# Optimization experiments

Hardware: AMD Instinct MI355X
Metric: run time of the kernel (lower is better)

The kernel has to match this reference:

```python
import jax, jax.numpy as jnp
import numpy as np

STATE_DIM = 4        # per-block state size (rel pos + rel vel, 2D)
N_NEIGH = 64         # neighbors per agent
BATCH = 4096         # observations in the batch (len(x) in torch code)
PHI_H, PHI_OUT = 256, 64
RHO_H, ACTION_DIM = 256, 2
R_AGENT = 0.15
A_MAX = 2.0


def setup_inputs() -> dict:
    key = jax.random.key(0)
    ks = jax.random.split(key, 5)

    def w(k, i, o):
        return jax.random.normal(k, (i, o), jnp.float32) / np.sqrt(i).astype(np.float32)

    x = jax.random.normal(ks[0], (BATCH, (N_NEIGH + 2) * STATE_DIM), jnp.float32)
    return dict(
        x=x,
        phi_w1=w(ks[1], STATE_DIM, PHI_H), phi_b1=jnp.zeros((PHI_H,), jnp.float32),
        phi_w2=w(ks[2], PHI_H, PHI_OUT), phi_b2=jnp.zeros((PHI_OUT,), jnp.float32),
        rho_w1=w(ks[3], PHI_OUT, RHO_H), rho_b1=jnp.zeros((RHO_H,), jnp.float32),
        rho_w2=w(ks[4], RHO_H, ACTION_DIM), rho_b2=jnp.zeros((ACTION_DIM,), jnp.float32),
    )


def reference(x, phi_w1, phi_b1, phi_w2, phi_b2, rho_w1, rho_b1, rho_w2, rho_b2):
    B = x.shape[0]
    blocks = x.reshape(B, -1, STATE_DIM)                 # [B, n_n+2, sd]
    # DeepSet: phi per block, permutation-invariant sum, rho head.
    h = jax.nn.relu(jnp.einsum('bns,sh->bnh', blocks, phi_w1) + phi_b1)
    phi = jnp.einsum('bnh,ho->bno', h, phi_w2) + phi_b2  # [B, n_n+2, phi_out]
    X = phi.sum(axis=1)                                  # [B, phi_out]
    h2 = jax.nn.relu(X @ rho_w1 + rho_b1)
    a = A_MAX * jnp.tanh(h2 @ rho_w2 + rho_b2)           # [B, action_dim]
    # Barrier: neighbor blocks start at block index 2; take first half (positions).
    p = blocks[:, 2:, : STATE_DIM // 2]                  # [B, n_n, 2]
    d = jnp.linalg.norm(p, axis=-1, keepdims=True)       # [B, n_n, 1]
    barrier = jnp.sum(-p / (d - R_AGENT) ** 2, axis=1)   # [B, 2]
    barrier = jax.lax.stop_gradient(barrier)  # torch goes through numpy -> detached
    a = a + barrier
    scale = A_MAX / jnp.max(a)  # torch.max(a_max)/torch.max(a_wbarrier), global max
    return jnp.where(scale < 1.0, a * scale, a)
```

## Files before the change

kernel.cpp:

```cpp
#include <hip/hip_runtime.h>
#include <math.h>


#define NBLK 1024

__global__ __launch_bounds__(256, 4) void bn_row(
    const float* __restrict__ x,
    const float* __restrict__ w1,  const float* __restrict__ b1,
    const float* __restrict__ w2,  const float* __restrict__ b2,
    const float* __restrict__ rw1, const float* __restrict__ rb1,
    const float* __restrict__ rw2, const float* __restrict__ rb2,
    float* __restrict__ out, float* __restrict__ blkmax)
{
    __shared__ __align__(16) float sx[4][268];
    __shared__ __align__(16) float sH[4][264];
    __shared__ float sXp[4][4][68];
    __shared__ __align__(16) float sX[4][68];
    __shared__ float sP4[4][4][2];
    __shared__ float sbar[4][2];
    __shared__ float sa[8];

    const int tid = threadIdx.x;
    const int ln  = tid & 63;
    const int wv  = tid >> 6;
    const int b0  = blockIdx.x * 4;
    const int row = b0 + wv;
    const float4* __restrict__ x4 = (const float4*)(x + (size_t)row * 264);

    float4 xr = x4[ln];
    float4 pv = x4[ln + 2];
    ((float4*)sx[wv])[ln] = xr;
    if (ln >= 62) ((float4*)sx[wv])[ln + 2] = pv;

    float4 w1r0 = ((const float4*)(w1      ))[ln];
    float4 w1r1 = ((const float4*)(w1 + 256))[ln];
    float4 w1r2 = ((const float4*)(w1 + 512))[ln];
    float4 w1r3 = ((const float4*)(w1 + 768))[ln];
    float4 b1r  = ((const float4*)b1)[ln];

    float a0 = 0.f, a1 = 0.f, a2 = 0.f, a3 = 0.f;
    #pragma unroll 4
    for (int n = 0; n < 66; n++) {
        float4 xv = ((const float4*)sx[wv])[n];
        float h0 = b1r.x, h1 = b1r.y, h2 = b1r.z, h3 = b1r.w;
        h0 = fmaf(xv.x, w1r0.x, h0); h1 = fmaf(xv.x, w1r0.y, h1);
        h2 = fmaf(xv.x, w1r0.z, h2); h3 = fmaf(xv.x, w1r0.w, h3);
        h0 = fmaf(xv.y, w1r1.x, h0); h1 = fmaf(xv.y, w1r1.y, h1);
        h2 = fmaf(xv.y, w1r1.z, h2); h3 = fmaf(xv.y, w1r1.w, h3);
        h0 = fmaf(xv.z, w1r2.x, h0); h1 = fmaf(xv.z, w1r2.y, h1);
        h2 = fmaf(xv.z, w1r2.z, h2); h3 = fmaf(xv.z, w1r2.w, h3);
        h0 = fmaf(xv.w, w1r3.x, h0); h1 = fmaf(xv.w, w1r3.y, h1);
        h2 = fmaf(xv.w, w1r3.z, h2); h3 = fmaf(xv.w, w1r3.w, h3);
        a0 += fmaxf(h0, 0.f); a1 += fmaxf(h1, 0.f);
        a2 += fmaxf(h2, 0.f); a3 += fmaxf(h3, 0.f);
    }
    ((float4*)sH[wv])[ln] = make_float4(a0, a1, a2, a3);

    {
        float px = pv.x, py = pv.y;
        float d  = sqrtf(px * px + py * py);
        float t  = d - 0.15f;
        float inv = 1.0f / (t * t);
        float bx = -px * inv, by = -py * inv;
        #pragma unroll
        for (int m = 32; m >= 1; m >>= 1) {
            bx += __shfl_xor(bx, m);
            by += __shfl_xor(by, m);
        }
        if (ln == 0) { sbar[wv][0] = bx; sbar[wv][1] = by; }
    }
    __syncthreads();

    {
        float xp0 = 0.f, xp1 = 0.f, xp2 = 0.f, xp3 = 0.f;
        const float* w2q = w2 + (wv << 12);
        #pragma unroll 2
        for (int i = 0; i < 16; i++) {
            int kb = (wv << 4) + i;
            float4 h0 = ((const float4*)sH[0])[kb];
            float4 h1 = ((const float4*)sH[1])[kb];
            float4 h2 = ((const float4*)sH[2])[kb];
            float4 h3 = ((const float4*)sH[3])[kb];
            float wk0 = w2q[(((i << 2) + 0) << 6) + ln];
            float wk1 = w2q[(((i << 2) + 1) << 6) + ln];
            float wk2 = w2q[(((i << 2) + 2) << 6) + ln];
            float wk3 = w2q[(((i << 2) + 3) << 6) + ln];
            xp0 = fmaf(h0.x, wk0, xp0); xp1 = fmaf(h1.x, wk0, xp1);
            xp2 = fmaf(h2.x, wk0, xp2); xp3 = fmaf(h3.x, wk0, xp3);
            xp0 = fmaf(h0.y, wk1, xp0); xp1 = fmaf(h1.y, wk1, xp1);
            xp2 = fmaf(h2.y, wk1, xp2); xp3 = fmaf(h3.y, wk1, xp3);
            xp0 = fmaf(h0.z, wk2, xp0); xp1 = fmaf(h1.z, wk2, xp1);
            xp2 = fmaf(h2.z, wk2, xp2); xp3 = fmaf(h3.z, wk2, xp3);
            xp0 = fmaf(h0.w, wk3, xp0); xp1 = fmaf(h1.w, wk3, xp1);
            xp2 = fmaf(h2.w, wk3, xp2); xp3 = fmaf(h3.w, wk3, xp3);
        }
        sXp[wv][0][ln] = xp0; sXp[wv][1][ln] = xp1;
        sXp[wv][2][ln] = xp2; sXp[wv][3][ln] = xp3;
    }
    __syncthreads();

    {
        float Xf = sXp[0][wv][ln] + sXp[1][wv][ln]
                 + sXp[2][wv][ln] + sXp[3][wv][ln] + 66.0f * b2[ln];
        sX[wv][ln] = Xf;
    }
    __syncthreads();

    float c0, c1, c2, c3;
    c0 = c1 = c2 = c3 = rb1[tid];
    #pragma unroll 2
    for (int i = 0; i < 16; i++) {
        float4 X0 = ((const float4*)sX[0])[i];
        float4 X1 = ((const float4*)sX[1])[i];
        float4 X2 = ((const float4*)sX[2])[i];
        float4 X3 = ((const float4*)sX[3])[i];
        float r0 = rw1[(((i << 2) + 0) << 8) + tid];
        float r1 = rw1[(((i << 2) + 1) << 8) + tid];
        float r2 = rw1[(((i << 2) + 2) << 8) + tid];
        float r3 = rw1[(((i << 2) + 3) << 8) + tid];
        c0 = fmaf(X0.x, r0, c0); c1 = fmaf(X1.x, r0, c1);
        c2 = fmaf(X2.x, r0, c2); c3 = fmaf(X3.x, r0, c3);
        c0 = fmaf(X0.y, r1, c0); c1 = fmaf(X1.y, r1, c1);
        c2 = fmaf(X2.y, r1, c2); c3 = fmaf(X3.y, r1, c3);
        c0 = fmaf(X0.z, r2, c0); c1 = fmaf(X1.z, r2, c1);
        c2 = fmaf(X2.z, r2, c2); c3 = fmaf(X3.z, r2, c3);
        c0 = fmaf(X0.w, r3, c0); c1 = fmaf(X1.w, r3, c1);
        c2 = fmaf(X2.w, r3, c2); c3 = fmaf(X3.w, r3, c3);
    }
    c0 = fmaxf(c0, 0.f); c1 = fmaxf(c1, 0.f);
    c2 = fmaxf(c2, 0.f); c3 = fmaxf(c3, 0.f);

    {
        float2 r2v = ((const float2*)rw2)[tid];
        float p00 = c0 * r2v.x, p01 = c0 * r2v.y;
        float p10 = c1 * r2v.x, p11 = c1 * r2v.y;
        float p20 = c2 * r2v.x, p21 = c2 * r2v.y;
        float p30 = c3 * r2v.x, p31 = c3 * r2v.y;
        #pragma unroll
        for (int m = 32; m >= 1; m >>= 1) {
            p00 += __shfl_xor(p00, m); p01 += __shfl_xor(p01, m);
            p10 += __shfl_xor(p10, m); p11 += __shfl_xor(p11, m);
            p20 += __shfl_xor(p20, m); p21 += __shfl_xor(p21, m);
            p30 += __shfl_xor(p30, m); p31 += __shfl_xor(p31, m);
        }
        if (ln == 0) {
            sP4[wv][0][0] = p00; sP4[wv][0][1] = p01;
            sP4[wv][1][0] = p10; sP4[wv][1][1] = p11;
            sP4[wv][2][0] = p20; sP4[wv][2][1] = p21;
            sP4[wv][3][0] = p30; sP4[wv][3][1] = p31;
        }
    }
    __syncthreads();

    if (tid < 8) {
        int r = tid >> 1, c = tid & 1;
        float pre = sP4[0][r][c] + sP4[1][r][c] + sP4[2][r][c] + sP4[3][r][c] + rb2[c];
        float a = 2.0f * tanhf(pre) + sbar[r][c];
        out[b0 * 2 + tid] = a;
        sa[tid] = a;
    }
    __syncthreads();
    if (tid == 0) {
        float m = sa[0];
        #pragma unroll
        for (int i = 1; i < 8; i++) m = fmaxf(m, sa[i]);
        blkmax[blockIdx.x] = m;
    }
}

__global__ __launch_bounds__(256) void bn_scale(
    float* __restrict__ out, const float* __restrict__ blkmax)
{
    __shared__ float sm[4];
    const int tid = threadIdx.x;
    const int ln  = tid & 63;
    const int wv  = tid >> 6;

    float m = fmaxf(fmaxf(blkmax[tid], blkmax[tid + 256]),
                    fmaxf(blkmax[tid + 512], blkmax[tid + 768]));
    #pragma unroll
    for (int s = 32; s >= 1; s >>= 1) m = fmaxf(m, __shfl_xor(m, s));
    if (ln == 0) sm[wv] = m;
    __syncthreads();
    float amax = fmaxf(fmaxf(sm[0], sm[1]), fmaxf(sm[2], sm[3]));

    float scale = 2.0f / amax;
    int i = blockIdx.x * 256 + tid;
    float a = out[i];
    out[i] = (scale < 1.0f) ? a * scale : a;
}

extern "C" void kernel_launch(void* const* d_in, const int* in_sizes, int n_in,
                              void* d_out, int out_size, void* d_ws, size_t ws_size,
                              hipStream_t stream) {
    const float* x   = (const float*)d_in[0];
    const float* w1  = (const float*)d_in[1];
    const float* b1  = (const float*)d_in[2];
    const float* w2  = (const float*)d_in[3];
    const float* b2  = (const float*)d_in[4];
    const float* rw1 = (const float*)d_in[5];
    const float* rb1 = (const float*)d_in[6];
    const float* rw2 = (const float*)d_in[7];
    const float* rb2 = (const float*)d_in[8];
    float* out = (float*)d_out;
    float* blkmax = (float*)d_ws;

    bn_row<<<NBLK, 256, 0, stream>>>(x, w1, b1, w2, b2, rw1, rb1, rw2, rb2,
                                     out, blkmax);
    bn_scale<<<8192 / 256, 256, 0, stream>>>(out, blkmax);
}
```

Measured before the change: 90.46 us.

## Split each row's phi loop across two waves, two rows per block

Each block now handles 2 rows instead of 4, and each row's 66-block phi layer-1 loop is split between two waves, with the partial sums combined in shared memory. This doubles the grid to 2048 blocks and raises the occupancy hint, cutting the per-wave serial loop length and the per-thread register footprint. The cost is an extra shared-memory reduction and barrier. The w2, rw1 and rw2 weights are also re-read by twice as many blocks, and the second kernel now reduces 2048 block maxima.

```diff
diff --git a/kernel.cpp b/kernel.cpp
--- a/kernel.cpp
+++ b/kernel.cpp
@@ -2,9 +2,9 @@
 #include <math.h>
 
 
-#define NBLK 1024
-
-__global__ __launch_bounds__(256, 4) void bn_row(
+#define NBLK 2048
+
+__global__ __launch_bounds__(256, 8) void bn_row(
     const float* __restrict__ x,
     const float* __restrict__ w1,  const float* __restrict__ b1,
     const float* __restrict__ w2,  const float* __restrict__ b2,
@@ -12,51 +12,62 @@
     const float* __restrict__ rw2, const float* __restrict__ rb2,
     float* __restrict__ out, float* __restrict__ blkmax)
 {
-    __shared__ __align__(16) float sx[4][268];
-    __shared__ __align__(16) float sH[4][264];
-    __shared__ float sXp[4][4][68];
-    __shared__ __align__(16) float sX[4][68];
-    __shared__ float sP4[4][4][2];
-    __shared__ float sbar[4][2];
-    __shared__ float sa[8];
+    __shared__ __align__(16) float sx[2][268];
+    __shared__ __align__(16) float sHp[4][264];
+    __shared__ __align__(16) float sH[2][264];
+    __shared__ float sXp[4][2][68];
+    __shared__ __align__(16) float sX[2][68];
+    __shared__ float sP4[4][2][2];
+    __shared__ float sbar[2][2];
+    __shared__ float sa[4];
 
     const int tid = threadIdx.x;
     const int ln  = tid & 63;
     const int wv  = tid >> 6;
-    const int b0  = blockIdx.x * 4;
-    const int row = b0 + wv;
+    const int p   = wv & 1;
+    const int rp  = wv >> 1;
+    const int r0  = blockIdx.x * 2;
+    const int row = r0 + rp;
     const float4* __restrict__ x4 = (const float4*)(x + (size_t)row * 264);
 
-    float4 xr = x4[ln];
-    float4 pv = x4[ln + 2];
-    ((float4*)sx[wv])[ln] = xr;
-    if (ln >= 62) ((float4*)sx[wv])[ln + 2] = pv;
+    float4 pv;
+    if (p == 0) {
+        float4 xr = x4[ln];
+        ((float4*)sx[rp])[ln] = xr;
+    } else {
+        pv = x4[ln + 2];
+        if (ln >= 62) ((float4*)sx[rp])[ln + 2] = pv;
+    }
 
     float4 w1r0 = ((const float4*)(w1      ))[ln];
     float4 w1r1 = ((const float4*)(w1 + 256))[ln];
     float4 w1r2 = ((const float4*)(w1 + 512))[ln];
     float4 w1r3 = ((const float4*)(w1 + 768))[ln];
     float4 b1r  = ((const float4*)b1)[ln];
+    __syncthreads();
 
     float a0 = 0.f, a1 = 0.f, a2 = 0.f, a3 = 0.f;
-    #pragma unroll 4
-    for (int n = 0; n < 66; n++) {
-        float4 xv = ((const float4*)sx[wv])[n];
-        float h0 = b1r.x, h1 = b1r.y, h2 = b1r.z, h3 = b1r.w;
-        h0 = fmaf(xv.x, w1r0.x, h0); h1 = fmaf(xv.x, w1r0.y, h1);
-        h2 = fmaf(xv.x, w1r0.z, h2); h3 = fmaf(xv.x, w1r0.w, h3);
-        h0 = fmaf(xv.y, w1r1.x, h0); h1 = fmaf(xv.y, w1r1.y, h1);
-        h2 = fmaf(xv.y, w1r1.z, h2); h3 = fmaf(xv.y, w1r1.w, h3);
-        h0 = fmaf(xv.z, w1r2.x, h0); h1 = fmaf(xv.z, w1r2.y, h1);
-        h2 = fmaf(xv.z, w1r2.z, h2); h3 = fmaf(xv.z, w1r2.w, h3);
-        h0 = fmaf(xv.w, w1r3.x, h0); h1 = fmaf(xv.w, w1r3.y, h1);
-        h2 = fmaf(xv.w, w1r3.z, h2); h3 = fmaf(xv.w, w1r3.w, h3);
-        a0 += fmaxf(h0, 0.f); a1 += fmaxf(h1, 0.f);
-        a2 += fmaxf(h2, 0.f); a3 += fmaxf(h3, 0.f);
-    }
-    ((float4*)sH[wv])[ln] = make_float4(a0, a1, a2, a3);
-
     {
+        const int nbeg = p * 33;
+        #pragma unroll 3
+        for (int j = 0; j < 33; j++) {
+            float4 xv = ((const float4*)sx[rp])[nbeg + j];
+            float h0 = b1r.x, h1 = b1r.y, h2 = b1r.z, h3 = b1r.w;
+            h0 = fmaf(xv.x, w1r0.x, h0); h1 = fmaf(xv.x, w1r0.y, h1);
+            h2 = fmaf(xv.x, w1r0.z, h2); h3 = fmaf(xv.x, w1r0.w, h3);
+            h0 = fmaf(xv.y, w1r1.x, h0); h1 = fmaf(xv.y, w1r1.y, h1);
+            h2 = fmaf(xv.y, w1r1.z, h2); h3 = fmaf(xv.y, w1r1.w, h3);
+            h0 = fmaf(xv.z, w1r2.x, h0); h1 = fmaf(xv.z, w1r2.y, h1);
+            h2 = fmaf(xv.z, w1r2.z, h2); h3 = fmaf(xv.z, w1r2.w, h3);
+            h0 = fmaf(xv.w, w1r3.x, h0); h1 = fmaf(xv.w, w1r3.y, h1);
+            h2 = fmaf(xv.w, w1r3.z, h2); h3 = fmaf(xv.w, w1r3.w, h3);
+            a0 += fmaxf(h0, 0.f); a1 += fmaxf(h1, 0.f);
+            a2 += fmaxf(h2, 0.f); a3 += fmaxf(h3, 0.f);
+        }
+    }
+    ((float4*)sHp[wv])[ln] = make_float4(a0, a1, a2, a3);
+
+    if (p == 1) {
         float px = pv.x, py = pv.y;
         float d  = sqrtf(px * px + py * py);
         float t  = d - 0.15f;
@@ -67,103 +78,87 @@
             bx += __shfl_xor(bx, m);
             by += __shfl_xor(by, m);
         }
-        if (ln == 0) { sbar[wv][0] = bx; sbar[wv][1] = by; }
+        if (ln == 0) { sbar[rp][0] = bx; sbar[rp][1] = by; }
+    }
+    __syncthreads();
+
+    for (int t = tid; t < 512; t += 256) {
+        int r = t >> 8, k = t & 255;
+        sH[r][k] = sHp[2 * r][k] + sHp[2 * r + 1][k];
     }
     __syncthreads();
 
     {
-        float xp0 = 0.f, xp1 = 0.f, xp2 = 0.f, xp3 = 0.f;
+        float xp0 = 0.f, xp1 = 0.f;
         const float* w2q = w2 + (wv << 12);
-        #pragma unroll 2
+        #pragma unroll 4
         for (int i = 0; i < 16; i++) {
             int kb = (wv << 4) + i;
             float4 h0 = ((const float4*)sH[0])[kb];
             float4 h1 = ((const float4*)sH[1])[kb];
-            float4 h2 = ((const float4*)sH[2])[kb];
-            float4 h3 = ((const float4*)sH[3])[kb];
             float wk0 = w2q[(((i << 2) + 0) << 6) + ln];
             float wk1 = w2q[(((i << 2) + 1) << 6) + ln];
             float wk2 = w2q[(((i << 2) + 2) << 6) + ln];
             float wk3 = w2q[(((i << 2) + 3) << 6) + ln];
             xp0 = fmaf(h0.x, wk0, xp0); xp1 = fmaf(h1.x, wk0, xp1);
-            xp2 = fmaf(h2.x, wk0, xp2); xp3 = fmaf(h3.x, wk0, xp3);
             xp0 = fmaf(h0.y, wk1, xp0); xp1 = fmaf(h1.y, wk1, xp1);
-            xp2 = fmaf(h2.y, wk1, xp2); xp3 = fmaf(h3.y, wk1, xp3);
             xp0 = fmaf(h0.z, wk2, xp0); xp1 = fmaf(h1.z, wk2, xp1);
-            xp2 = fmaf(h2.z, wk2, xp2); xp3 = fmaf(h3.z, wk2, xp3);
             xp0 = fmaf(h0.w, wk3, xp0); xp1 = fmaf(h1.w, wk3, xp1);
-            xp2 = fmaf(h2.w, wk3, xp2); xp3 = fmaf(h3.w, wk3, xp3);
         }
         sXp[wv][0][ln] = xp0; sXp[wv][1][ln] = xp1;
-        sXp[wv][2][ln] = xp2; sXp[wv][3][ln] = xp3;
-    }
-    __syncthreads();
-
-    {
-        float Xf = sXp[0][wv][ln] + sXp[1][wv][ln]
-                 + sXp[2][wv][ln] + sXp[3][wv][ln] + 66.0f * b2[ln];
-        sX[wv][ln] = Xf;
-    }
-    __syncthreads();
-
-    float c0, c1, c2, c3;
-    c0 = c1 = c2 = c3 = rb1[tid];
-    #pragma unroll 2
+    }
+    __syncthreads();
+
+    if (wv < 2) {
+        sX[wv][ln] = sXp[0][wv][ln] + sXp[1][wv][ln]
+                   + sXp[2][wv][ln] + sXp[3][wv][ln] + 66.0f * b2[ln];
+    }
+    __syncthreads();
+
+    float c0, c1;
+    c0 = c1 = rb1[tid];
+    #pragma unroll 4
     for (int i = 0; i < 16; i++) {
         float4 X0 = ((const float4*)sX[0])[i];
         float4 X1 = ((const float4*)sX[1])[i];
-        float4 X2 = ((const float4*)sX[2])[i];
-        float4 X3 = ((const float4*)sX[3])[i];
-        float r0 = rw1[(((i << 2) + 0) << 8) + tid];
-        float r1 = rw1[(((i << 2) + 1) << 8) + tid];
-        float r2 = rw1[(((i << 2) + 2) << 8) + tid];
-        float r3 = rw1[(((i << 2) + 3) << 8) + tid];
-        c0 = fmaf(X0.x, r0, c0); c1 = fmaf(X1.x, r0, c1);
-        c2 = fmaf(X2.x, r0, c2); c3 = fmaf(X3.x, r0, c3);
-        c0 = fmaf(X0.y, r1, c0); c1 = fmaf(X1.y, r1, c1);
-        c2 = fmaf(X2.y, r1, c2); c3 = fmaf(X3.y, r1, c3);
-        c0 = fmaf(X0.z, r2, c0); c1 = fmaf(X1.z, r2, c1);
-        c2 = fmaf(X2.z, r2, c2); c3 = fmaf(X3.z, r2, c3);
-        c0 = fmaf(X0.w, r3, c0); c1 = fmaf(X1.w, r3, c1);
-        c2 = fmaf(X2.w, r3, c2); c3 = fmaf(X3.w, r3, c3);
+        float q0 = rw1[(((i << 2) + 0) << 8) + tid];
+        float q1 = rw1[(((i << 2) + 1) << 8) + tid];
+        float q2 = rw1[(((i << 2) + 2) << 8) + tid];
+        float q3 = rw1[(((i << 2) + 3) << 8) + tid];
+        c0 = fmaf(X0.x, q0, c0); c1 = fmaf(X1.x, q0, c1);
+        c0 = fmaf(X0.y, q1, c0); c1 = fmaf(X1.y, q1, c1);
+        c0 = fmaf(X0.z, q2, c0); c1 = fmaf(X1.z, q2, c1);
+        c0 = fmaf(X0.w, q3, c0); c1 = fmaf(X1.w, q3, c1);
     }
     c0 = fmaxf(c0, 0.f); c1 = fmaxf(c1, 0.f);
-    c2 = fmaxf(c2, 0.f); c3 = fmaxf(c3, 0.f);
 
     {
         float2 r2v = ((const float2*)rw2)[tid];
         float p00 = c0 * r2v.x, p01 = c0 * r2v.y;
         float p10 = c1 * r2v.x, p11 = c1 * r2v.y;
-        float p20 = c2 * r2v.x, p21 = c2 * r2v.y;
-        float p30 = c3 * r2v.x, p31 = c3 * r2v.y;
         #pragma unroll
         for (int m = 32; m >= 1; m >>= 1) {
             p00 += __shfl_xor(p00, m); p01 += __shfl_xor(p01, m);
             p10 += __shfl_xor(p10, m); p11 += __shfl_xor(p11, m);
-            p20 += __shfl_xor(p20, m); p21 += __shfl_xor(p21, m);
-            p30 += __shfl_xor(p30, m); p31 += __shfl_xor(p31, m);
         }
         if (ln == 0) {
             sP4[wv][0][0] = p00; sP4[wv][0][1] = p01;
             sP4[wv][1][0] = p10; sP4[wv][1][1] = p11;
-            sP4[wv][2][0] = p20; sP4[wv][2][1] = p21;
-            sP4[wv][3][0] = p30; sP4[wv][3][1] = p31;
-        }
-    }
-    __syncthreads();
-
-    if (tid < 8) {
+        }
+    }
+    __syncthreads();
+
+    if (tid < 4) {
         int r = tid >> 1, c = tid & 1;
-        float pre = sP4[0][r][c] + sP4[1][r][c] + sP4[2][r][c] + sP4[3][r][c] + rb2[c];
+        float pre = sP4[0][r][c] + sP4[1][r][c] + sP4[2][r][c] + sP4[3][r][c]
+                  + rb2[c];
         float a = 2.0f * tanhf(pre) + sbar[r][c];
-        out[b0 * 2 + tid] = a;
+        out[r0 * 2 + tid] = a;
         sa[tid] = a;
     }
     __syncthreads();
     if (tid == 0) {
-        float m = sa[0];
-        #pragma unroll
-        for (int i = 1; i < 8; i++) m = fmaxf(m, sa[i]);
+        float m = fmaxf(fmaxf(sa[0], sa[1]), fmaxf(sa[2], sa[3]));
         blkmax[blockIdx.x] = m;
     }
 }
@@ -176,8 +171,9 @@
     const int ln  = tid & 63;
     const int wv  = tid >> 6;
 
-    float m = fmaxf(fmaxf(blkmax[tid], blkmax[tid + 256]),
-                    fmaxf(blkmax[tid + 512], blkmax[tid + 768]));
+    float m = blkmax[tid];
+    #pragma unroll
+    for (int j = 1; j < 8; j++) m = fmaxf(m, blkmax[tid + 256 * j]);
     #pragma unroll
     for (int s = 32; s >= 1; s >>= 1) m = fmaxf(m, __shfl_xor(m, s));
     if (ln == 0) sm[wv] = m;
```

Measured after the change: 91.67 us. About the same (+1.3%).
